# Kernel tuning notes

Hardware: AMD Instinct MI355X
Metric: run time of the kernel (lower is better)

The kernel has to match this reference:

```python
import jax, jax.numpy as jnp
import numpy as np

N_EMBD = 1024
N_HEADS = 16
HEAD_DIM = N_EMBD // N_HEADS


def setup_inputs() -> dict:
    key = jax.random.key(0)
    ks = jax.random.split(key, 6)
    s = 1.0 / np.sqrt(N_EMBD)
    x = jax.random.normal(ks[0], (2, 2048, N_EMBD), dtype=jnp.float32)
    # torch Linear weights are [out, in]; y = x @ W.T
    Wk = jax.random.uniform(ks[1], (N_EMBD, N_EMBD), jnp.float32, -s, s)
    Wq = jax.random.uniform(ks[2], (N_EMBD, N_EMBD), jnp.float32, -s, s)
    Wv = jax.random.uniform(ks[3], (N_EMBD, N_EMBD), jnp.float32, -s, s)
    Wp = jax.random.uniform(ks[4], (N_EMBD, N_EMBD), jnp.float32, -s, s)
    bp = jax.random.uniform(ks[5], (N_EMBD,), jnp.float32, -s, s)
    return {"x": x, "Wq": Wq, "Wk": Wk, "Wv": Wv, "Wp": Wp, "bp": bp}


def reference(x, Wq, Wk, Wv, Wp, bp):
    B, T, C = x.shape
    H, D = N_HEADS, HEAD_DIM
    # projections (torch Linear: x @ W.T), reshape to [B, H, T, D]
    q = (x @ Wq.T).reshape(B, T, H, D).transpose(0, 2, 1, 3)
    k = (x @ Wk.T).reshape(B, T, H, D).transpose(0, 2, 1, 3)
    v = (x @ Wv.T).reshape(B, T, H, D).transpose(0, 2, 1, 3)
    # scaled causal attention, full [B,H,T,T] scores (faithful to original)
    att = jnp.einsum('bhqd,bhkd->bhqk', q, k) * (D ** -0.5)
    causal = jnp.tril(jnp.ones((T, T), dtype=bool))
    att = jnp.where(causal[None, None], att, -jnp.inf)
    att = jax.nn.softmax(att, axis=-1)
    out = jnp.einsum('bhqk,bhkd->bhqd', att, v)
    out = out.transpose(0, 2, 1, 3).reshape(B, T, C)
    return out @ Wp.T + bp
```

## Files before the change

kernel.cpp:

```cpp
#include <hip/hip_runtime.h>

typedef __bf16 bf16;
typedef __bf16 bf16x8 __attribute__((ext_vector_type(8)));
typedef float f32x4 __attribute__((ext_vector_type(4)));

typedef __attribute__((address_space(1))) const void as1_void;
typedef __attribute__((address_space(3))) void as3_void;

#define DEV __device__ __forceinline__
#define NEG_BIG (-1.0e30f)


DEV void async_load16(const void* g, void* l) {
  __builtin_amdgcn_global_load_lds((as1_void*)g, (as3_void*)l, 16, 0, 0);
}
DEV bf16x8 load8(const bf16* p) { bf16x8 v; __builtin_memcpy(&v, p, 16); return v; }
DEV void store8(bf16* p, bf16x8 v) { __builtin_memcpy(p, &v, 16); }

DEV int sniff_bf16(const unsigned short* __restrict__ xr) {
  const int lane = threadIdx.x & 63;
  const unsigned short w = xr[lane * 2];
  const int e = (w >> 7) & 0xFF;
  const bool sane = ((w & 0x7FFF) == 0) || (e >= 97 && e <= 157);
  return __popcll(__ballot(sane)) >= 48;
}

struct ConvArgs {
  const void* src[6];
  bf16* dst[6];
  int n[6];
};

__global__ __launch_bounds__(256) void convert_kernel(ConvArgs a) {
  const int isbf = sniff_bf16((const unsigned short*)a.src[0]);
  const int t = blockIdx.y;
  const int n = a.n[t];
  bf16* d = a.dst[t];
  const int stride = gridDim.x * 256 * 8;
  if (isbf) {
    const bf16* s = (const bf16*)a.src[t];
    for (int i = (blockIdx.x * 256 + threadIdx.x) * 8; i < n; i += stride)
      store8(d + i, load8(s + i));
  } else {
    const float* s = (const float*)a.src[t];
    for (int i = (blockIdx.x * 256 + threadIdx.x) * 8; i < n; i += stride) {
      float tmp[8];
      __builtin_memcpy(tmp, s + i, 32);
      bf16x8 v;
#pragma unroll
      for (int j = 0; j < 8; ++j) v[j] = (bf16)tmp[j];
      store8(d + i, v);
    }
  }
}

DEV void gemm_core_128_p(const bf16* A, const bf16* W, const int K, int m0, int n0,
                         f32x4 (&acc)[4][4]) {
  __shared__ alignas(16) bf16 As[3][128 * 32];
  __shared__ alignas(16) bf16 Bs[3][128 * 32];
  const int tid = threadIdx.x;
  const int lane = tid & 63;
  const int wid = tid >> 6;
  const int wm = (wid >> 1) << 6;
  const int wn = (wid & 1) << 6;
  const int lr = lane & 15;
  const int lg = lane >> 4;

  size_t srcA[2], srcB[2];
  int ldsoff[2];
#pragma unroll
  for (int it = 0; it < 2; ++it) {
    const int lin = it * 256 + tid;
    const int lr2 = lin >> 3, c = lin & 7;
    const int u = c ^ (lr2 & 7);
    const int r = lr2 * 2 + (u >> 2);
    const int g = u & 3;
    srcA[it] = (size_t)(m0 + r) * K + (size_t)(g * 8);
    srcB[it] = (size_t)(n0 + r) * K + (size_t)(g * 8);
    ldsoff[it] = lin * 8;
  }
  int offA[4], offB[4];
#pragma unroll
  for (int i = 0; i < 4; ++i) {
    const int r = wm + i * 16 + lr;
    const int cc = (lg | ((r & 1) << 2)) ^ ((r >> 1) & 7);
    offA[i] = (((r >> 1) << 3) | cc) * 8;
  }
#pragma unroll
  for (int j = 0; j < 4; ++j) {
    const int r = wn + j * 16 + lr;
    const int cc = (lg | ((r & 1) << 2)) ^ ((r >> 1) & 7);
    offB[j] = (((r >> 1) << 3) | cc) * 8;
  }

  const f32x4 zero = {0.f, 0.f, 0.f, 0.f};
#pragma unroll
  for (int i = 0; i < 4; ++i)
#pragma unroll
    for (int j = 0; j < 4; ++j) acc[i][j] = zero;

  const int nt = K >> 5;

  auto stage = [&](int buf, int t) {
    const size_t k0 = (size_t)(t << 5);
#pragma unroll
    for (int it = 0; it < 2; ++it) {
      async_load16(A + srcA[it] + k0, &As[buf][0] + ldsoff[it]);
      async_load16(W + srcB[it] + k0, &Bs[buf][0] + ldsoff[it]);
    }
  };

  auto compute = [&](int buf) {
    const bf16* as = &As[buf][0];
    const bf16* bs = &Bs[buf][0];
    bf16x8 af[4], bfr[4];
#pragma unroll
    for (int i = 0; i < 4; ++i) af[i] = load8(as + offA[i]);
#pragma unroll
    for (int j = 0; j < 4; ++j) bfr[j] = load8(bs + offB[j]);
    __builtin_amdgcn_s_setprio(1);
#pragma unroll
    for (int i = 0; i < 4; ++i)
#pragma unroll
      for (int j = 0; j < 4; ++j)
        acc[i][j] = __builtin_amdgcn_mfma_f32_16x16x32_bf16(af[i], bfr[j], acc[i][j], 0, 0, 0);
    __builtin_amdgcn_s_setprio(0);
  };

  stage(0, 0);
  stage(1, 1);
  int b0 = 0, b1 = 1, b2 = 2;
  for (int t = 0; t < nt; ++t) {
    if (t + 1 < nt) asm volatile("s_waitcnt vmcnt(4)" ::: "memory");
    else            asm volatile("s_waitcnt vmcnt(0)" ::: "memory");
    __builtin_amdgcn_s_barrier();
    if (t + 2 < nt) stage(b2, t + 2);
    compute(b0);
    const int tmp = b0; b0 = b1; b1 = b2; b2 = tmp;
  }
}

DEV size_t frag_idx(int row, int col) {
  return ((size_t)(((col >> 5) * 4 + ((row >> 4) & 3)) * 64 + ((col >> 3) & 3) * 16 + (row & 15)) << 3)
         | (size_t)(col & 7);
}

__global__ __launch_bounds__(256) void qkv_proj_kernel(
    const bf16* __restrict__ x, const bf16* __restrict__ Wq,
    const bf16* __restrict__ Wk, const bf16* __restrict__ Wv,
    bf16* __restrict__ q_ws, bf16* __restrict__ k_ws, bf16* __restrict__ vt_ws) {
  const int L = blockIdx.x;
  const int xcd = L & 7;
  const int i2 = L >> 3;
  const int m0 = (xcd * 4 + (i2 & 3)) << 7;
  const int rest = i2 >> 2;
  const int n0 = (rest & 7) << 7;
  const int mode = rest >> 3;
  const bf16* W = (mode == 0) ? Wq : (mode == 1) ? Wk : Wv;
  f32x4 acc[4][4];
  gemm_core_128_p(x, W, 1024, m0, n0, acc);

  const int tid = threadIdx.x;
  const int lane = tid & 63, wid = tid >> 6;
  const int wm = (wid >> 1) << 6, wn = (wid & 1) << 6;
  const int lr = lane & 15, lg = lane >> 4;
  bf16* out = (mode == 0) ? q_ws : (mode == 1) ? k_ws : vt_ws;
#pragma unroll
  for (int i = 0; i < 4; ++i) {
#pragma unroll
    for (int r = 0; r < 4; ++r) {
      const int m = m0 + wm + i * 16 + lg * 4 + r;
      const int b = m >> 11, t = m & 2047;
#pragma unroll
      for (int j = 0; j < 4; ++j) {
        const int n = n0 + wn + j * 16 + lr;
        const int h = n >> 6, d = n & 63;
        const float v = acc[i][j][r];
        const size_t base = ((size_t)(b * 16 + h) << 17) + ((size_t)(t >> 6) << 12);
        const size_t idx = base + ((mode < 2) ? frag_idx(t & 63, d) : frag_idx(d, t & 63));
        out[idx] = (bf16)v;
      }
    }
  }
}

__global__ __launch_bounds__(256, 2) void attn_kernel(
    const bf16* __restrict__ q_ws, const bf16* __restrict__ k_ws,
    const bf16* __restrict__ vt_ws, bf16* __restrict__ a_ws) {
  const int L = blockIdx.x;
  const int xcd = L & 7;
  const int bh = xcd * 4 + ((L >> 3) & 3);
  const int qt = 31 - (L >> 5);
  const int tid = threadIdx.x;
  const int lane = tid & 63, w = tid >> 6;
  const int lr = lane & 15, lg = lane >> 4;
  const int fo = lg * 16 + lr;

  __shared__ alignas(16) bf16 Ks[3][4096];
  __shared__ alignas(16) bf16 Vs[3][4096];
  __shared__ alignas(16) bf16 Ps[4][16 * 72];
  bf16* ps = &Ps[w][0];

  const size_t hb = (size_t)bh << 17;
  const int b = bh >> 4, h = bh & 15;
  const f32x4 zero = {0.f, 0.f, 0.f, 0.f};

  const size_t qtb = hb + ((size_t)qt << 12);
  const bf16* kbase = k_ws + hb;
  const bf16* vbase = vt_ws + hb;

  bf16x8 aq[2];
#pragma unroll
  for (int c2 = 0; c2 < 2; ++c2)
    aq[c2] = load8(q_ws + qtb + (size_t)(((c2 * 4 + w) * 64 + fo) << 3));

  f32x4 o_acc[4];
#pragma unroll
  for (int j = 0; j < 4; ++j) o_acc[j] = zero;
  float lsum[4] = {0.f, 0.f, 0.f, 0.f};

  const int nt = qt + 1;
  auto ktof = [&](int s) { return (s == 0) ? qt : (s - 1); };

  auto stage = [&](int buf, int s) {
    const int kt = ktof(s);
    const bf16* kg = kbase + ((size_t)kt << 12);
    const bf16* vg = vbase + ((size_t)kt << 12);
#pragma unroll
    for (int it = 0; it < 2; ++it) {
      const int lin = it * 256 + tid;
      async_load16(kg + lin * 8, &Ks[buf][0] + lin * 8);
      async_load16(vg + lin * 8, &Vs[buf][0] + lin * 8);
    }
  };

  auto step = [&](int buf, bool diag) {
    const bf16* ks = &Ks[buf][0];
    const bf16* vs = &Vs[buf][0];
    f32x4 s[4];
    __builtin_amdgcn_s_setprio(1);
#pragma unroll
    for (int j = 0; j < 4; ++j) {
      s[j] = __builtin_amdgcn_mfma_f32_16x16x32_bf16(
          aq[0], load8(ks + (size_t)(((0 * 4 + j) * 64 + fo) << 3)), zero, 0, 0, 0);
      s[j] = __builtin_amdgcn_mfma_f32_16x16x32_bf16(
          aq[1], load8(ks + (size_t)(((1 * 4 + j) * 64 + fo) << 3)), s[j], 0, 0, 0);
    }
    __builtin_amdgcn_s_setprio(0);
    float p[4][4];
#pragma unroll
    for (int j = 0; j < 4; ++j) {
#pragma unroll
      for (int r = 0; r < 4; ++r) {
        float v = s[j][r] * 0.125f;
        if (diag && (j * 16 + lr) > (w * 16 + lg * 4 + r)) v = NEG_BIG;
        p[j][r] = __expf(v);
      }
    }
#pragma unroll
    for (int r = 0; r < 4; ++r)
      lsum[r] += (p[0][r] + p[1][r]) + (p[2][r] + p[3][r]);
#pragma unroll
    for (int j = 0; j < 4; ++j)
#pragma unroll
      for (int r = 0; r < 4; ++r)
        ps[(lg * 4 + r) * 72 + j * 16 + lr] = (bf16)p[j][r];
    __builtin_amdgcn_s_setprio(1);
#pragma unroll
    for (int c2 = 0; c2 < 2; ++c2) {
      const bf16x8 ap = load8(ps + lr * 72 + c2 * 32 + lg * 8);
#pragma unroll
      for (int j = 0; j < 4; ++j)
        o_acc[j] = __builtin_amdgcn_mfma_f32_16x16x32_bf16(
            ap, load8(vs + (size_t)(((c2 * 4 + j) * 64 + fo) << 3)), o_acc[j], 0, 0, 0);
    }
    __builtin_amdgcn_s_setprio(0);
  };

  stage(0, 0);
  if (nt > 1) stage(1, 1);
  int b0 = 0, b1 = 1, b2 = 2;
  for (int t = 0; t < nt; ++t) {
    if (t + 1 < nt) asm volatile("s_waitcnt vmcnt(4)" ::: "memory");
    else            asm volatile("s_waitcnt vmcnt(0)" ::: "memory");
    __builtin_amdgcn_s_barrier();
    if (t + 2 < nt) stage(b2, t + 2);
    step(b0, t == 0);
    const int tmp = b0; b0 = b1; b1 = b2; b2 = tmp;
  }

  float l_i[4];
#pragma unroll
  for (int r = 0; r < 4; ++r) {
    float v = lsum[r];
#pragma unroll
    for (int off = 1; off < 16; off <<= 1) v += __shfl_xor(v, off, 64);
    l_i[r] = v;
  }

#pragma unroll
  for (int r = 0; r < 4; ++r) {
    const int t = qt * 64 + w * 16 + lg * 4 + r;
    const float inv = 1.f / l_i[r];
#pragma unroll
    for (int j = 0; j < 4; ++j) {
      const size_t idx = (((size_t)(b * 2048 + t)) << 10) | (size_t)(h * 64 + j * 16 + lr);
      a_ws[idx] = (bf16)(o_acc[j][r] * inv);
    }
  }
}

__global__ __launch_bounds__(256) void out_proj_kernel(
    const bf16* __restrict__ A, const bf16* __restrict__ Wp,
    const bf16* __restrict__ bp, void* __restrict__ out,
    const unsigned short* __restrict__ xraw) {
  const int L = blockIdx.x;
  const int xcd = L & 7;
  const int i2 = L >> 3;
  const int m0 = (xcd * 4 + (i2 & 3)) << 7;
  const int n0 = (i2 >> 2) << 7;
  f32x4 acc[4][4];
  gemm_core_128_p(A, Wp, 1024, m0, n0, acc);

  const int tid = threadIdx.x;
  const int lane = tid & 63, wid = tid >> 6;
  const int wm = (wid >> 1) << 6, wn = (wid & 1) << 6;
  const int lr = lane & 15, lg = lane >> 4;
  const int isbf = sniff_bf16(xraw);
#pragma unroll
  for (int i = 0; i < 4; ++i) {
#pragma unroll
    for (int r = 0; r < 4; ++r) {
      const int m = m0 + wm + i * 16 + lg * 4 + r;
#pragma unroll
      for (int j = 0; j < 4; ++j) {
        const int n = n0 + wn + j * 16 + lr;
        const float v = acc[i][j][r] + (float)bp[n];
        const size_t idx = ((size_t)m << 10) | (size_t)n;
        if (isbf) ((bf16*)out)[idx] = (bf16)v;
        else      ((float*)out)[idx] = v;
      }
    }
  }
}

extern "C" void kernel_launch(void* const* d_in, const int* in_sizes, int n_in,
                              void* d_out, int out_size, void* d_ws, size_t ws_size,
                              hipStream_t stream) {
  (void)in_sizes; (void)n_in; (void)out_size;
  if (ws_size < (50u << 20)) return;

  char* ws = (char*)d_ws;
  bf16* q_ws  = (bf16*)(ws);
  bf16* k_ws  = (bf16*)(ws + (8u << 20));
  bf16* vt_ws = (bf16*)(ws + (16u << 20));
  bf16* a_ws  = (bf16*)(ws + (24u << 20));
  bf16* xc    = (bf16*)(ws + (32u << 20));
  bf16* Wqc   = (bf16*)(ws + (40u << 20));
  bf16* Wkc   = (bf16*)(ws + (42u << 20));
  bf16* Wvc   = (bf16*)(ws + (44u << 20));
  bf16* Wpc   = (bf16*)(ws + (46u << 20));
  bf16* bpc   = (bf16*)(ws + (48u << 20));

  ConvArgs ca;
  ca.src[0] = d_in[0]; ca.dst[0] = xc;  ca.n[0] = 4096 * 1024;
  ca.src[1] = d_in[1]; ca.dst[1] = Wqc; ca.n[1] = 1024 * 1024;
  ca.src[2] = d_in[2]; ca.dst[2] = Wkc; ca.n[2] = 1024 * 1024;
  ca.src[3] = d_in[3]; ca.dst[3] = Wvc; ca.n[3] = 1024 * 1024;
  ca.src[4] = d_in[4]; ca.dst[4] = Wpc; ca.n[4] = 1024 * 1024;
  ca.src[5] = d_in[5]; ca.dst[5] = bpc; ca.n[5] = 1024;
  convert_kernel<<<dim3(512, 6), 256, 0, stream>>>(ca);

  qkv_proj_kernel<<<768, 256, 0, stream>>>(xc, Wqc, Wkc, Wvc, q_ws, k_ws, vt_ws);
  attn_kernel<<<1024, 256, 0, stream>>>(q_ws, k_ws, vt_ws, a_ws);
  out_proj_kernel<<<256, 256, 0, stream>>>(a_ws, Wpc, bpc, d_out,
                                           (const unsigned short*)d_in[0]);
}
```

Baseline: 184.9 us.

## Process two query tiles per attention block and fold softmax scale into Q

Each attention block now handles two adjacent 64-row query tiles and shares every staged K/V tile between them, which halves the grid to 512 blocks and halves K/V global traffic per query. The softmax scale and log2(e) are folded into Q during the QKV projection, so the attention loop can call raw v_exp_f32 (exp2) without a per-element multiply. In exchange there are fewer blocks to fill the GPU and more registers per thread for the doubled accumulators and preloaded K/V fragments. Masked steps are also still computed, since the second tile's final key tile is processed with a full mask for the first tile.

```diff
diff --git a/kernel.cpp b/kernel.cpp
--- a/kernel.cpp
+++ b/kernel.cpp
@@ -16,6 +16,7 @@
 }
 DEV bf16x8 load8(const bf16* p) { bf16x8 v; __builtin_memcpy(&v, p, 16); return v; }
 DEV void store8(bf16* p, bf16x8 v) { __builtin_memcpy(p, &v, 16); }
+DEV float fexp2(float x) { float r; asm("v_exp_f32 %0, %1" : "=v"(r) : "v"(x)); return r; }
 
 DEV int sniff_bf16(const unsigned short* __restrict__ xr) {
   const int lane = threadIdx.x & 63;
@@ -165,6 +166,7 @@
   const int wm = (wid >> 1) << 6, wn = (wid & 1) << 6;
   const int lr = lane & 15, lg = lane >> 4;
   bf16* out = (mode == 0) ? q_ws : (mode == 1) ? k_ws : vt_ws;
+  const float scale = (mode == 0) ? 0.18033688011112042f : 1.0f;
 #pragma unroll
   for (int i = 0; i < 4; ++i) {
 #pragma unroll
@@ -175,7 +177,7 @@
       for (int j = 0; j < 4; ++j) {
         const int n = n0 + wn + j * 16 + lr;
         const int h = n >> 6, d = n & 63;
-        const float v = acc[i][j][r];
+        const float v = acc[i][j][r] * scale;
         const size_t base = ((size_t)(b * 16 + h) << 17) + ((size_t)(t >> 6) << 12);
         const size_t idx = base + ((mode < 2) ? frag_idx(t & 63, d) : frag_idx(d, t & 63));
         out[idx] = (bf16)v;
@@ -188,9 +190,8 @@
     const bf16* __restrict__ q_ws, const bf16* __restrict__ k_ws,
     const bf16* __restrict__ vt_ws, bf16* __restrict__ a_ws) {
   const int L = blockIdx.x;
-  const int xcd = L & 7;
-  const int bh = xcd * 4 + ((L >> 3) & 3);
-  const int qt = 31 - (L >> 5);
+  const int bh = (L & 7) * 4 + ((L >> 3) & 3);
+  const int qt2 = 15 - (L >> 5);
   const int tid = threadIdx.x;
   const int lane = tid & 63, w = tid >> 6;
   const int lr = lane & 15, lg = lane >> 4;
@@ -205,25 +206,28 @@
   const int b = bh >> 4, h = bh & 15;
   const f32x4 zero = {0.f, 0.f, 0.f, 0.f};
 
-  const size_t qtb = hb + ((size_t)qt << 12);
   const bf16* kbase = k_ws + hb;
   const bf16* vbase = vt_ws + hb;
 
-  bf16x8 aq[2];
-#pragma unroll
-  for (int c2 = 0; c2 < 2; ++c2)
-    aq[c2] = load8(q_ws + qtb + (size_t)(((c2 * 4 + w) * 64 + fo) << 3));
-
-  f32x4 o_acc[4];
-#pragma unroll
-  for (int j = 0; j < 4; ++j) o_acc[j] = zero;
-  float lsum[4] = {0.f, 0.f, 0.f, 0.f};
-
-  const int nt = qt + 1;
-  auto ktof = [&](int s) { return (s == 0) ? qt : (s - 1); };
-
-  auto stage = [&](int buf, int s) {
-    const int kt = ktof(s);
+  bf16x8 aq[2][2];
+#pragma unroll
+  for (int s = 0; s < 2; ++s) {
+    const size_t qtb = hb + ((size_t)(qt2 * 2 + s) << 12);
+#pragma unroll
+    for (int c2 = 0; c2 < 2; ++c2)
+      aq[s][c2] = load8(q_ws + qtb + (size_t)(((c2 * 4 + w) * 64 + fo) << 3));
+  }
+
+  f32x4 o_acc[2][4];
+  float lsum[2][4];
+#pragma unroll
+  for (int s = 0; s < 2; ++s)
+#pragma unroll
+    for (int j = 0; j < 4; ++j) { o_acc[s][j] = zero; lsum[s][j] = 0.f; }
+
+  const int nk = 2 * qt2 + 2;
+
+  auto stage = [&](int buf, int kt) {
     const bf16* kg = kbase + ((size_t)kt << 12);
     const bf16* vg = vbase + ((size_t)kt << 12);
 #pragma unroll
@@ -234,78 +238,94 @@
     }
   };
 
-  auto step = [&](int buf, bool diag) {
+  auto step = [&](int buf, int t) {
     const bf16* ks = &Ks[buf][0];
     const bf16* vs = &Vs[buf][0];
-    f32x4 s[4];
-    __builtin_amdgcn_s_setprio(1);
-#pragma unroll
-    for (int j = 0; j < 4; ++j) {
-      s[j] = __builtin_amdgcn_mfma_f32_16x16x32_bf16(
-          aq[0], load8(ks + (size_t)(((0 * 4 + j) * 64 + fo) << 3)), zero, 0, 0, 0);
-      s[j] = __builtin_amdgcn_mfma_f32_16x16x32_bf16(
-          aq[1], load8(ks + (size_t)(((1 * 4 + j) * 64 + fo) << 3)), s[j], 0, 0, 0);
-    }
-    __builtin_amdgcn_s_setprio(0);
-    float p[4][4];
-#pragma unroll
-    for (int j = 0; j < 4; ++j) {
-#pragma unroll
-      for (int r = 0; r < 4; ++r) {
-        float v = s[j][r] * 0.125f;
-        if (diag && (j * 16 + lr) > (w * 16 + lg * 4 + r)) v = NEG_BIG;
-        p[j][r] = __expf(v);
-      }
-    }
-#pragma unroll
-    for (int r = 0; r < 4; ++r)
-      lsum[r] += (p[0][r] + p[1][r]) + (p[2][r] + p[3][r]);
-#pragma unroll
-    for (int j = 0; j < 4; ++j)
+    f32x4 sv[2][4];
+    {
+      bf16x8 kf[2][4];
+#pragma unroll
+      for (int c2 = 0; c2 < 2; ++c2)
+#pragma unroll
+        for (int j = 0; j < 4; ++j)
+          kf[c2][j] = load8(ks + (size_t)(((c2 * 4 + j) * 64 + fo) << 3));
+      __builtin_amdgcn_s_setprio(1);
+#pragma unroll
+      for (int s = 0; s < 2; ++s)
+#pragma unroll
+        for (int j = 0; j < 4; ++j) {
+          sv[s][j] = __builtin_amdgcn_mfma_f32_16x16x32_bf16(aq[s][0], kf[0][j], zero, 0, 0, 0);
+          sv[s][j] = __builtin_amdgcn_mfma_f32_16x16x32_bf16(aq[s][1], kf[1][j], sv[s][j], 0, 0, 0);
+        }
+      __builtin_amdgcn_s_setprio(0);
+    }
+    bf16x8 vf[2][4];
+#pragma unroll
+    for (int c2 = 0; c2 < 2; ++c2)
+#pragma unroll
+      for (int j = 0; j < 4; ++j)
+        vf[c2][j] = load8(vs + (size_t)(((c2 * 4 + j) * 64 + fo) << 3));
+
+#pragma unroll
+    for (int s = 0; s < 2; ++s) {
+      const int rel = t - 2 * qt2 - s;
+      float p[4][4];
+#pragma unroll
+      for (int j = 0; j < 4; ++j) {
+#pragma unroll
+        for (int r = 0; r < 4; ++r) {
+          float v = sv[s][j][r];
+          if (rel == 0 && (j * 16 + lr) > (w * 16 + lg * 4 + r)) v = NEG_BIG;
+          if (rel > 0) v = NEG_BIG;
+          p[j][r] = fexp2(v);
+        }
+      }
 #pragma unroll
       for (int r = 0; r < 4; ++r)
-        ps[(lg * 4 + r) * 72 + j * 16 + lr] = (bf16)p[j][r];
-    __builtin_amdgcn_s_setprio(1);
-#pragma unroll
-    for (int c2 = 0; c2 < 2; ++c2) {
-      const bf16x8 ap = load8(ps + lr * 72 + c2 * 32 + lg * 8);
+        lsum[s][r] += (p[0][r] + p[1][r]) + (p[2][r] + p[3][r]);
 #pragma unroll
       for (int j = 0; j < 4; ++j)
-        o_acc[j] = __builtin_amdgcn_mfma_f32_16x16x32_bf16(
-            ap, load8(vs + (size_t)(((c2 * 4 + j) * 64 + fo) << 3)), o_acc[j], 0, 0, 0);
-    }
-    __builtin_amdgcn_s_setprio(0);
+#pragma unroll
+        for (int r = 0; r < 4; ++r)
+          ps[(lg * 4 + r) * 72 + j * 16 + lr] = (bf16)p[j][r];
+      __builtin_amdgcn_s_setprio(1);
+#pragma unroll
+      for (int c2 = 0; c2 < 2; ++c2) {
+        const bf16x8 ap = load8(ps + lr * 72 + c2 * 32 + lg * 8);
+#pragma unroll
+        for (int j = 0; j < 4; ++j)
+          o_acc[s][j] = __builtin_amdgcn_mfma_f32_16x16x32_bf16(ap, vf[c2][j], o_acc[s][j], 0, 0, 0);
+      }
+      __builtin_amdgcn_s_setprio(0);
+    }
   };
 
   stage(0, 0);
-  if (nt > 1) stage(1, 1);
+  stage(1, 1);
   int b0 = 0, b1 = 1, b2 = 2;
-  for (int t = 0; t < nt; ++t) {
-    if (t + 1 < nt) asm volatile("s_waitcnt vmcnt(4)" ::: "memory");
+  for (int t = 0; t < nk; ++t) {
+    if (t + 1 < nk) asm volatile("s_waitcnt vmcnt(4)" ::: "memory");
     else            asm volatile("s_waitcnt vmcnt(0)" ::: "memory");
     __builtin_amdgcn_s_barrier();
-    if (t + 2 < nt) stage(b2, t + 2);
-    step(b0, t == 0);
+    if (t + 2 < nk) stage(b2, t + 2);
+    step(b0, t);
     const int tmp = b0; b0 = b1; b1 = b2; b2 = tmp;
   }
 
-  float l_i[4];
-#pragma unroll
-  for (int r = 0; r < 4; ++r) {
-    float v = lsum[r];
-#pragma unroll
-    for (int off = 1; off < 16; off <<= 1) v += __shfl_xor(v, off, 64);
-    l_i[r] = v;
-  }
-
-#pragma unroll
-  for (int r = 0; r < 4; ++r) {
-    const int t = qt * 64 + w * 16 + lg * 4 + r;
-    const float inv = 1.f / l_i[r];
-#pragma unroll
-    for (int j = 0; j < 4; ++j) {
-      const size_t idx = (((size_t)(b * 2048 + t)) << 10) | (size_t)(h * 64 + j * 16 + lr);
-      a_ws[idx] = (bf16)(o_acc[j][r] * inv);
+#pragma unroll
+  for (int s = 0; s < 2; ++s) {
+#pragma unroll
+    for (int r = 0; r < 4; ++r) {
+      float v = lsum[s][r];
+#pragma unroll
+      for (int off = 1; off < 16; off <<= 1) v += __shfl_xor(v, off, 64);
+      const float inv = 1.f / v;
+      const int t = qt2 * 128 + s * 64 + w * 16 + lg * 4 + r;
+#pragma unroll
+      for (int j = 0; j < 4; ++j) {
+        const size_t idx = (((size_t)(b * 2048 + t)) << 10) | (size_t)(h * 64 + j * 16 + lr);
+        a_ws[idx] = (bf16)(o_acc[s][j][r] * inv);
+      }
     }
   }
 }
@@ -372,7 +392,7 @@
   convert_kernel<<<dim3(512, 6), 256, 0, stream>>>(ca);
 
   qkv_proj_kernel<<<768, 256, 0, stream>>>(xc, Wqc, Wkc, Wvc, q_ws, k_ws, vt_ws);
-  attn_kernel<<<1024, 256, 0, stream>>>(q_ws, k_ws, vt_ws, a_ws);
+  attn_kernel<<<512, 256, 0, stream>>>(q_ws, k_ws, vt_ws, a_ws);
   out_proj_kernel<<<256, 256, 0, stream>>>(a_ws, Wpc, bpc, d_out,
                                            (const unsigned short*)d_in[0]);
 }
```

After: 194.0 us. 1.05x slower.
